# Kernel tuning notes

Measured on AMD Instinct MI355X. Metric: run time of the kernel, lower is better.

The kernel has to match this reference:

```python
import math
import jax, jax.numpy as jnp
import numpy as np

B, LD, LE = 8, 512, 512
D, H, DK, F, L, V = 1024, 16, 64, 4096, 3, 32000
EPS = 1e-5
NEG = -1000000000.0


def setup_inputs() -> dict:
    key = jax.random.key(0)
    ks = jax.random.split(key, 16)
    s = 0.02
    dec_inputs = jax.random.randint(ks[0], (B, LD), 0, V)
    # causal mask: True = masked out (matches masked_fill semantics)
    self_mask = jnp.broadcast_to(jnp.triu(jnp.ones((LD, LD), bool), k=1), (B, LD, LD))
    enc_output = jax.random.normal(ks[1], (B, LE, D), jnp.float32)
    encoder_mask = jnp.zeros((B, LD, LE), bool)  # no encoder padding
    embed = jax.random.normal(ks[2], (V, D), jnp.float32) * s
    # sinusoidal positional encoding, pe[:LD]
    pos = jnp.arange(LD, dtype=jnp.float32)[:, None]
    div = jnp.exp(jnp.arange(0, D, 2, dtype=jnp.float32) * (-math.log(10000.0) / D))
    pe = jnp.zeros((LD, D), jnp.float32)
    pe = pe.at[:, 0::2].set(jnp.sin(pos * div)).at[:, 1::2].set(jnp.cos(pos * div))
    # per-layer params; axis 1 of attn params: 0=self-attn, 1=enc-dec attn
    wq = jax.random.normal(ks[3], (L, 2, D, D), jnp.float32) * s
    wk = jax.random.normal(ks[4], (L, 2, D, D), jnp.float32) * s
    wv = jax.random.normal(ks[5], (L, 2, D, D), jnp.float32) * s
    wo = jax.random.normal(ks[6], (L, 2, D, D), jnp.float32) * s
    bq = jnp.zeros((L, 2, D), jnp.float32)
    bk = jnp.zeros((L, 2, D), jnp.float32)
    bv = jnp.zeros((L, 2, D), jnp.float32)
    bo = jnp.zeros((L, 2, D), jnp.float32)
    ffn_w1 = jax.random.normal(ks[7], (L, F, D), jnp.float32) * s
    ffn_b1 = jnp.zeros((L, F), jnp.float32)
    ffn_w2 = jax.random.normal(ks[8], (L, D, F), jnp.float32) * s
    ffn_b2 = jnp.zeros((L, D), jnp.float32)
    ln_g = jnp.ones((L, 3, D), jnp.float32)   # norm1/2/3 gains
    ln_b = jnp.zeros((L, 3, D), jnp.float32)  # norm1/2/3 biases
    return dict(dec_inputs=dec_inputs, self_mask=self_mask, enc_output=enc_output,
                encoder_mask=encoder_mask, embed=embed, pe=pe,
                wq=wq, bq=bq, wk=wk, bk=bk, wv=wv, bv=bv, wo=wo, bo=bo,
                ffn_w1=ffn_w1, ffn_b1=ffn_b1, ffn_w2=ffn_w2, ffn_b2=ffn_b2,
                ln_g=ln_g, ln_b=ln_b)


def _ln(x, g, b):
    m = jnp.mean(x, axis=-1, keepdims=True)
    v = jnp.mean((x - m) ** 2, axis=-1, keepdims=True)
    return (x - m) * jax.lax.rsqrt(v + EPS) * g + b


def _mha(qi, ki, vi, mask, wq, bq, wk, bk, wv, bv, wo, bo):
    Bq, Lq, _ = qi.shape
    Lk = ki.shape[1]
    Q = (qi @ wq.T + bq).reshape(Bq, Lq, H, DK).transpose(0, 2, 1, 3)
    K = (ki @ wk.T + bk).reshape(Bq, Lk, H, DK).transpose(0, 2, 1, 3)
    Vv = (vi @ wv.T + bv).reshape(Bq, Lk, H, DK).transpose(0, 2, 1, 3)
    scores = jnp.einsum('bhqd,bhkd->bhqk', Q, K) / math.sqrt(DK)
    scores = jnp.where(mask[:, None, :, :], NEG, scores)
    attn = jax.nn.softmax(scores, axis=-1)
    ctx = jnp.einsum('bhqk,bhkd->bhqd', attn, Vv)
    ctx = ctx.transpose(0, 2, 1, 3).reshape(Bq, Lq, H * DK)
    return ctx @ wo.T + bo


def reference(dec_inputs, self_mask, enc_output, encoder_mask, embed, pe,
              wq, bq, wk, bk, wv, bv, wo, bo,
              ffn_w1, ffn_b1, ffn_w2, ffn_b2, ln_g, ln_b):
    x = embed[dec_inputs] * math.sqrt(D) + pe[None, :, :]
    for l in range(L):
        h = _ln(x, ln_g[l, 0], ln_b[l, 0])
        a = _mha(h, h, h, self_mask,
                 wq[l, 0], bq[l, 0], wk[l, 0], bk[l, 0], wv[l, 0], bv[l, 0], wo[l, 0], bo[l, 0])
        x = x + a
        h = _ln(x, ln_g[l, 1], ln_b[l, 1])
        c = _mha(h, enc_output, enc_output, encoder_mask,
                 wq[l, 1], bq[l, 1], wk[l, 1], bk[l, 1], wv[l, 1], bv[l, 1], wo[l, 1], bo[l, 1])
        x = x + c
        h = _ln(x, ln_g[l, 2], ln_b[l, 2])
        f = jax.nn.relu(h @ ffn_w1[l].T + ffn_b1[l]) @ ffn_w2[l].T + ffn_b2[l]
        # faithful quirk of the source: residual is the cross-attn output, not x
        x = c + f
    return x
```

## Files before the change

### kernel.cpp

```cpp
#include <hip/hip_runtime.h>
#include <hip/hip_bf16.h>

using bf16x8 = __attribute__((ext_vector_type(8))) short;
using f32x4  = __attribute__((ext_vector_type(4))) float;
using u16x4  = __attribute__((ext_vector_type(4))) unsigned short;

#define DEVI static __device__ __forceinline__

DEVI unsigned short f2b(float f) {
  unsigned int u = __float_as_uint(f);
  u += 0x7FFFu + ((u >> 16) & 1u);
  return (unsigned short)(u >> 16);
}

DEVI void gload16(const unsigned short* g, unsigned short* l) {
  __builtin_amdgcn_global_load_lds(
      (const __attribute__((address_space(1))) unsigned int*)g,
      (__attribute__((address_space(3))) unsigned int*)l, 16, 0, 0);
}

DEVI float wred_max16(float v) {
#pragma unroll
  for (int m = 1; m < 16; m <<= 1) v = fmaxf(v, __shfl_xor(v, m, 64));
  return v;
}
DEVI float wred_sum16(float v) {
#pragma unroll
  for (int m = 1; m < 16; m <<= 1) v += __shfl_xor(v, m, 64);
  return v;
}


__global__ void cvt_kernel(const float* __restrict__ in,
                           unsigned short* __restrict__ out, int n4) {
  int i = blockIdx.x * blockDim.x + threadIdx.x;
  const int stride = gridDim.x * blockDim.x;
  for (; i < n4; i += stride) {
    const float4 v = ((const float4*)in)[i];
    u16x4 o;
    o[0] = f2b(v.x); o[1] = f2b(v.y); o[2] = f2b(v.z); o[3] = f2b(v.w);
    ((u16x4*)out)[i] = o;
  }
}

__global__ void pack_w(const float* __restrict__ s0,
                       const float* __restrict__ s1,
                       const float* __restrict__ s2,
                       int sub, unsigned short* __restrict__ dst, int nm) {
  const int r = blockIdx.x;
  const int m = blockIdx.y;
  const int l = blockIdx.z;
  const float* src = (m == 0 ? s0 : m == 1 ? s1 : s2)
                   + (size_t)(l * 2 + sub) * 1048576 + (size_t)r * 1024;
  unsigned short* d = dst + ((size_t)(l * nm + m) * 1024 + r) * 1024;
  const int col = threadIdx.x * 4;
  const float4 v = *(const float4*)(src + col);
  u16x4 o;
  o[0] = f2b(v.x); o[1] = f2b(v.y); o[2] = f2b(v.z); o[3] = f2b(v.w);
  *(u16x4*)(d + col) = o;
}

__global__ void pack_bias(const float* __restrict__ s0,
                          const float* __restrict__ s1,
                          const float* __restrict__ s2,
                          int sub, float* __restrict__ dst, int nm) {
  const int m = blockIdx.x, l = blockIdx.y;
  const float* src = (m == 0 ? s0 : m == 1 ? s1 : s2) + (size_t)(l * 2 + sub) * 1024;
  float* d = dst + ((size_t)l * nm + m) * 1024;
  const int i = threadIdx.x * 4;
  *(float4*)(d + i) = *(const float4*)(src + i);
}

__global__ void embed_kernel(const int* __restrict__ ids,
                             const float* __restrict__ emb,
                             const float* __restrict__ pe,
                             float* __restrict__ x) {
  const int row = blockIdx.x;
  const int t = row & 511;
  const int col = threadIdx.x * 4;
  const int id = ids[row];
  const float4 e = *(const float4*)(emb + (size_t)id * 1024 + col);
  const float4 p = *(const float4*)(pe + (size_t)t * 1024 + col);
  float4 o;
  o.x = e.x * 32.f + p.x; o.y = e.y * 32.f + p.y;
  o.z = e.z * 32.f + p.z; o.w = e.w * 32.f + p.w;
  *(float4*)(x + (size_t)row * 1024 + col) = o;
}

__global__ void ln_kernel(const float* __restrict__ x,
                          const float* __restrict__ g,
                          const float* __restrict__ b,
                          unsigned short* __restrict__ out) {
  const int row = blockIdx.x;
  const int l = threadIdx.x;
  const float4* xr = (const float4*)(x + (size_t)row * 1024);
  float4 v[4];
  float s = 0.f;
#pragma unroll
  for (int i = 0; i < 4; ++i) {
    v[i] = xr[l * 4 + i];
    s += v[i].x + v[i].y + v[i].z + v[i].w;
  }
#pragma unroll
  for (int m = 1; m < 64; m <<= 1) s += __shfl_xor(s, m, 64);
  const float mean = s * (1.f / 1024.f);
  float vs = 0.f;
#pragma unroll
  for (int i = 0; i < 4; ++i) {
    float dx = v[i].x - mean, dy = v[i].y - mean, dz = v[i].z - mean, dw = v[i].w - mean;
    vs += dx * dx + dy * dy + dz * dz + dw * dw;
  }
#pragma unroll
  for (int m = 1; m < 64; m <<= 1) vs += __shfl_xor(vs, m, 64);
  const float inv = rsqrtf(vs * (1.f / 1024.f) + 1e-5f);
#pragma unroll
  for (int i = 0; i < 4; ++i) {
    const int col = l * 16 + i * 4;
    const float4 gg = *(const float4*)(g + col);
    const float4 bb = *(const float4*)(b + col);
    u16x4 o;
    o[0] = f2b((v[i].x - mean) * inv * gg.x + bb.x);
    o[1] = f2b((v[i].y - mean) * inv * gg.y + bb.y);
    o[2] = f2b((v[i].z - mean) * inv * gg.z + bb.z);
    o[3] = f2b((v[i].w - mean) * inv * gg.w + bb.w);
    *(u16x4*)(out + (size_t)row * 1024 + col) = o;
  }
}


enum { EPI_BF16 = 0, EPI_RELU_BF16 = 1, EPI_RES = 2, EPI_RES2 = 3 };

template<int EPI>
__global__ void gemm_bt(const unsigned short* __restrict__ A,
                        const unsigned short* __restrict__ Bw,
                        const float* __restrict__ bias,
                        int N, int K, int nn,
                        void* out0, const float* res, float* out1) {
  __shared__ alignas(16) unsigned short As[2][64 * 64];
  __shared__ alignas(16) unsigned short Bs[2][128 * 64];
  const int tid = threadIdx.x;
  const int lane = tid & 63;
  const int wave = tid >> 6;
  int id = blockIdx.x;
  const int nwg = gridDim.x;
  id = (id & 7) * (nwg >> 3) + (id >> 3);
  const int bx = id % nn;
  const int by = id / nn;
  const int m0 = by * 64;
  const int n0 = bx * 128;
  const int wm = (wave >> 1) * 32;
  const int wn = (wave & 1) * 64;

  auto stage = [&](int buf, int kt) {
    const size_t k0 = (size_t)kt * 64;
#pragma unroll
    for (int i = 0; i < 2; ++i) {
      const int c = tid + 256 * i;
      const int row = c >> 3;
      const int lc = (c & 7) ^ (row & 7);
      gload16(A + (size_t)(m0 + row) * K + k0 + lc * 8, &As[buf][c * 8]);
    }
#pragma unroll
    for (int i = 0; i < 4; ++i) {
      const int c = tid + 256 * i;
      const int row = c >> 3;
      const int lc = (c & 7) ^ (row & 7);
      gload16(Bw + (size_t)(n0 + row) * K + k0 + lc * 8, &Bs[buf][c * 8]);
    }
  };

  f32x4 acc[2][4];
#pragma unroll
  for (int i = 0; i < 2; ++i)
#pragma unroll
    for (int j = 0; j < 4; ++j) acc[i][j] = f32x4{0.f, 0.f, 0.f, 0.f};

  const int nk = K >> 6;
  stage(0, 0);
  int cur = 0;
  const int ro = lane & 15;
  const int hi = lane >> 4;
  for (int kt = 0; kt < nk; ++kt) {
    __syncthreads();
    if (kt + 1 < nk) stage(cur ^ 1, kt + 1);
    bf16x8 af[2][2], bf[4][2];
#pragma unroll
    for (int i = 0; i < 2; ++i) {
      const int r = wm + i * 16 + ro;
#pragma unroll
      for (int ks = 0; ks < 2; ++ks)
        af[i][ks] = *(const bf16x8*)&As[cur][r * 64 + (((ks << 2) + hi) ^ (r & 7)) * 8];
    }
#pragma unroll
    for (int j = 0; j < 4; ++j) {
      const int r = wn + j * 16 + ro;
#pragma unroll
      for (int ks = 0; ks < 2; ++ks)
        bf[j][ks] = *(const bf16x8*)&Bs[cur][r * 64 + (((ks << 2) + hi) ^ (r & 7)) * 8];
    }
#pragma unroll
    for (int ks = 0; ks < 2; ++ks)
#pragma unroll
      for (int i = 0; i < 2; ++i)
#pragma unroll
        for (int j = 0; j < 4; ++j)
          acc[i][j] = __builtin_amdgcn_mfma_f32_16x16x32_bf16(af[i][ks], bf[j][ks], acc[i][j], 0, 0, 0);
    cur ^= 1;
  }

  const int r4 = hi * 4;
#pragma unroll
  for (int i = 0; i < 2; ++i) {
#pragma unroll
    for (int j = 0; j < 4; ++j) {
      const int cg = n0 + wn + j * 16 + ro;
      const float bv = bias[cg];
#pragma unroll
      for (int q = 0; q < 4; ++q) {
        const int rg = m0 + wm + i * 16 + r4 + q;
        const size_t idx = (size_t)rg * N + cg;
        const float v = acc[i][j][q] + bv;
        if (EPI == EPI_BF16) {
          ((unsigned short*)out0)[idx] = f2b(v);
        } else if (EPI == EPI_RELU_BF16) {
          ((unsigned short*)out0)[idx] = f2b(fmaxf(v, 0.f));
        } else if (EPI == EPI_RES) {
          ((float*)out0)[idx] = res[idx] + v;
        } else {
          const float r = res[idx];
          ((float*)out0)[idx] = v;
          out1[idx] = r + v;
        }
      }
    }
  }
}


template<bool CAUSAL>
__global__ __launch_bounds__(64) void attn_kernel(
    const unsigned short* __restrict__ Qg, int qs,
    const unsigned short* __restrict__ Kg, int ksd,
    const unsigned short* __restrict__ Vg, int vsd,
    unsigned short* __restrict__ Og) {
  __shared__ alignas(16) unsigned short Pl[64 * 64];
  const int qt = blockIdx.x;
  const int h  = blockIdx.y;
  const int b  = blockIdx.z;
  const int lane = threadIdx.x;
  const int ro = lane & 15;
  const int hi = lane >> 4;
  const size_t qbase = (size_t)b * 512 * qs  + (size_t)h * 64;
  const size_t kbase = (size_t)b * 512 * ksd + (size_t)h * 64;
  const size_t vbase = (size_t)b * 512 * vsd + (size_t)h * 64;
  const size_t obase = (size_t)b * 512 * 1024 + (size_t)h * 64;

  bf16x8 qf[4][2];
#pragma unroll
  for (int mi = 0; mi < 4; ++mi)
#pragma unroll
    for (int ks = 0; ks < 2; ++ks)
      qf[mi][ks] = *(const bf16x8*)&Qg[qbase + (size_t)(qt * 64 + mi * 16 + ro) * qs + ks * 32 + hi * 8];

  f32x4 o[4][4];
  float mrun[4][4], lrun[4][4];
#pragma unroll
  for (int mi = 0; mi < 4; ++mi) {
#pragma unroll
    for (int di = 0; di < 4; ++di) o[mi][di] = f32x4{0.f, 0.f, 0.f, 0.f};
#pragma unroll
    for (int q = 0; q < 4; ++q) { mrun[mi][q] = -1e30f; lrun[mi][q] = 0.f; }
  }

  const int ktmax = CAUSAL ? qt : 7;
  for (int kt = 0; kt <= ktmax; ++kt) {
    bf16x8 kf[4][2];
#pragma unroll
    for (int ni = 0; ni < 4; ++ni)
#pragma unroll
      for (int ks = 0; ks < 2; ++ks)
        kf[ni][ks] = *(const bf16x8*)&Kg[kbase + (size_t)(kt * 64 + ni * 16 + ro) * ksd + ks * 32 + hi * 8];

    f32x4 s[4][4];
#pragma unroll
    for (int mi = 0; mi < 4; ++mi)
#pragma unroll
      for (int ni = 0; ni < 4; ++ni) s[mi][ni] = f32x4{0.f, 0.f, 0.f, 0.f};
#pragma unroll
    for (int ks = 0; ks < 2; ++ks)
#pragma unroll
      for (int mi = 0; mi < 4; ++mi)
#pragma unroll
        for (int ni = 0; ni < 4; ++ni)
          s[mi][ni] = __builtin_amdgcn_mfma_f32_16x16x32_bf16(qf[mi][ks], kf[ni][ks], s[mi][ni], 0, 0, 0);

#pragma unroll
    for (int mi = 0; mi < 4; ++mi)
#pragma unroll
      for (int ni = 0; ni < 4; ++ni)
#pragma unroll
        for (int q = 0; q < 4; ++q) {
          float e = s[mi][ni][q] * 0.125f;
          if (CAUSAL && kt == qt && (ni * 16 + ro) > (mi * 16 + hi * 4 + q)) e = -1e9f;
          s[mi][ni][q] = e;
        }

    float fac[4][4];
#pragma unroll
    for (int mi = 0; mi < 4; ++mi)
#pragma unroll
      for (int q = 0; q < 4; ++q) {
        float rm = s[mi][0][q];
#pragma unroll
        for (int ni = 1; ni < 4; ++ni) rm = fmaxf(rm, s[mi][ni][q]);
        rm = wred_max16(rm);
        const float mn = fmaxf(mrun[mi][q], rm);
        fac[mi][q] = __expf(mrun[mi][q] - mn);
        mrun[mi][q] = mn;
      }
#pragma unroll
    for (int mi = 0; mi < 4; ++mi)
#pragma unroll
      for (int q = 0; q < 4; ++q) {
        float rs = 0.f;
#pragma unroll
        for (int ni = 0; ni < 4; ++ni) {
          const float pv = __expf(s[mi][ni][q] - mrun[mi][q]);
          s[mi][ni][q] = pv;
          rs += pv;
        }
        rs = wred_sum16(rs);
        lrun[mi][q] = lrun[mi][q] * fac[mi][q] + rs;
      }
#pragma unroll
    for (int mi = 0; mi < 4; ++mi)
#pragma unroll
      for (int di = 0; di < 4; ++di)
#pragma unroll
        for (int q = 0; q < 4; ++q) o[mi][di][q] *= fac[mi][q];

#pragma unroll
    for (int mi = 0; mi < 4; ++mi)
#pragma unroll
      for (int ni = 0; ni < 4; ++ni)
#pragma unroll
        for (int q = 0; q < 4; ++q)
          Pl[(mi * 16 + hi * 4 + q) * 64 + ni * 16 + ro] = f2b(s[mi][ni][q]);

    bf16x8 pa[4][2];
#pragma unroll
    for (int mi = 0; mi < 4; ++mi)
#pragma unroll
      for (int ks = 0; ks < 2; ++ks)
        pa[mi][ks] = *(const bf16x8*)&Pl[(mi * 16 + ro) * 64 + ks * 32 + hi * 8];

#pragma unroll
    for (int di = 0; di < 4; ++di)
#pragma unroll
      for (int ks = 0; ks < 2; ++ks) {
        bf16x8 vf;
#pragma unroll
        for (int jj = 0; jj < 8; ++jj)
          vf[jj] = (short)Vg[vbase + (size_t)(kt * 64 + ks * 32 + hi * 8 + jj) * vsd + di * 16 + ro];
#pragma unroll
        for (int mi = 0; mi < 4; ++mi)
          o[mi][di] = __builtin_amdgcn_mfma_f32_16x16x32_bf16(pa[mi][ks], vf, o[mi][di], 0, 0, 0);
      }
  }

#pragma unroll
  for (int mi = 0; mi < 4; ++mi)
#pragma unroll
    for (int di = 0; di < 4; ++di)
#pragma unroll
      for (int q = 0; q < 4; ++q) {
        const float val = o[mi][di][q] / lrun[mi][q];
        Og[obase + (size_t)(qt * 64 + mi * 16 + hi * 4 + q) * 1024 + di * 16 + ro] = f2b(val);
      }
}


extern "C" void kernel_launch(void* const* d_in, const int* in_sizes, int n_in,
                              void* d_out, int out_size, void* d_ws, size_t ws_size,
                              hipStream_t stream) {
  (void)in_sizes; (void)n_in; (void)out_size; (void)ws_size;
  const int*   dec = (const int*)d_in[0];
  const float* enc = (const float*)d_in[2];
  const float* emb = (const float*)d_in[4];
  const float* pe  = (const float*)d_in[5];
  const float* wq  = (const float*)d_in[6];
  const float* bq  = (const float*)d_in[7];
  const float* wk  = (const float*)d_in[8];
  const float* bk  = (const float*)d_in[9];
  const float* wv  = (const float*)d_in[10];
  const float* bv  = (const float*)d_in[11];
  const float* wo  = (const float*)d_in[12];
  const float* bo  = (const float*)d_in[13];
  const float* w1  = (const float*)d_in[14];
  const float* b1  = (const float*)d_in[15];
  const float* w2  = (const float*)d_in[16];
  const float* b2  = (const float*)d_in[17];
  const float* lng = (const float*)d_in[18];
  const float* lnb = (const float*)d_in[19];

  const size_t SZ_ACT = 4194304ull;

  char* p = (char*)d_ws;
  auto alloc = [&](size_t bytes) { char* r = p; p += (bytes + 255) & ~(size_t)255; return r; };
  unsigned short* qkvw  = (unsigned short*)alloc(3ull * 3 * 1048576 * 2);
  unsigned short* kvw   = (unsigned short*)alloc(3ull * 2 * 1048576 * 2);
  unsigned short* wqxb  = (unsigned short*)alloc(3ull * 1048576 * 2);
  unsigned short* Wob   = (unsigned short*)alloc(6291456ull * 2);
  unsigned short* W1b   = (unsigned short*)alloc(12582912ull * 2);
  unsigned short* W2b   = (unsigned short*)alloc(12582912ull * 2);
  unsigned short* encb  = (unsigned short*)alloc(SZ_ACT * 2);
  float*          x     = (float*)alloc(SZ_ACT * 4);
  float*          c     = (float*)alloc(SZ_ACT * 4);
  unsigned short* hb    = (unsigned short*)alloc(SZ_ACT * 2);
  unsigned short* qkvb  = (unsigned short*)alloc(4096ull * 3072 * 2);
  unsigned short* kvb   = (unsigned short*)alloc(4096ull * 2048 * 2);
  unsigned short* qb    = (unsigned short*)alloc(SZ_ACT * 2);
  unsigned short* mid   = (unsigned short*)alloc(4096ull * 4096 * 2);
  float*          qkvbias = (float*)alloc(3ull * 3072 * 4);
  float*          kvbias  = (float*)alloc(3ull * 2048 * 4);

  cvt_kernel<<<2048, 256, 0, stream>>>(wo, Wob, 1572864);
  cvt_kernel<<<2048, 256, 0, stream>>>(w1, W1b, 3145728);
  cvt_kernel<<<2048, 256, 0, stream>>>(w2, W2b, 3145728);
  cvt_kernel<<<2048, 256, 0, stream>>>(enc, encb, 1048576);
  pack_w<<<dim3(1024, 3, 3), 256, 0, stream>>>(wq, wk, wv, 0, qkvw, 3);
  pack_w<<<dim3(1024, 2, 3), 256, 0, stream>>>(wk, wv, wv, 1, kvw, 2);
  pack_w<<<dim3(1024, 1, 3), 256, 0, stream>>>(wq, wq, wq, 1, wqxb, 1);
  pack_bias<<<dim3(3, 3), 256, 0, stream>>>(bq, bk, bv, 0, qkvbias, 3);
  pack_bias<<<dim3(2, 3), 256, 0, stream>>>(bk, bv, bv, 1, kvbias, 2);
  embed_kernel<<<4096, 256, 0, stream>>>(dec, emb, pe, x);

  const dim3 gAttn(8, 16, 8);

  for (int l = 0; l < 3; ++l) {
    const float* g0 = lng + (l * 3 + 0) * 1024; const float* e0 = lnb + (l * 3 + 0) * 1024;
    const float* g1 = lng + (l * 3 + 1) * 1024; const float* e1 = lnb + (l * 3 + 1) * 1024;
    const float* g2 = lng + (l * 3 + 2) * 1024; const float* e2 = lnb + (l * 3 + 2) * 1024;

    ln_kernel<<<4096, 64, 0, stream>>>(x, g0, e0, hb);
    gemm_bt<EPI_BF16><<<64 * 24, 256, 0, stream>>>(hb, qkvw + (size_t)l * 3 * 1048576,
        qkvbias + l * 3072, 3072, 1024, 24, qkvb, nullptr, nullptr);
    attn_kernel<true><<<gAttn, 64, 0, stream>>>(qkvb, 3072, qkvb + 1024, 3072,
                                                qkvb + 2048, 3072, hb);
    gemm_bt<EPI_RES><<<64 * 8, 256, 0, stream>>>(hb, Wob + (size_t)(l * 2) * 1048576,
        bo + (l * 2) * 1024, 1024, 1024, 8, x, x, nullptr);

    ln_kernel<<<4096, 64, 0, stream>>>(x, g1, e1, hb);
    gemm_bt<EPI_BF16><<<64 * 8, 256, 0, stream>>>(hb, wqxb + (size_t)l * 1048576,
        bq + (l * 2 + 1) * 1024, 1024, 1024, 8, qb, nullptr, nullptr);
    gemm_bt<EPI_BF16><<<64 * 16, 256, 0, stream>>>(encb, kvw + (size_t)l * 2 * 1048576,
        kvbias + l * 2048, 2048, 1024, 16, kvb, nullptr, nullptr);
    attn_kernel<false><<<gAttn, 64, 0, stream>>>(qb, 1024, kvb, 2048, kvb + 1024, 2048, hb);
    gemm_bt<EPI_RES2><<<64 * 8, 256, 0, stream>>>(hb, Wob + (size_t)(l * 2 + 1) * 1048576,
        bo + (l * 2 + 1) * 1024, 1024, 1024, 8, c, x, x);

    ln_kernel<<<4096, 64, 0, stream>>>(x, g2, e2, hb);
    gemm_bt<EPI_RELU_BF16><<<64 * 32, 256, 0, stream>>>(hb, W1b + (size_t)l * 4194304,
        b1 + l * 4096, 4096, 1024, 32, mid, nullptr, nullptr);
    float* xout = (l == 2) ? (float*)d_out : x;
    gemm_bt<EPI_RES><<<64 * 8, 256, 0, stream>>>(mid, W2b + (size_t)l * 4194304,
        b2 + l * 1024, 1024, 4096, 8, xout, c, nullptr);
  }
}
```

Measured before the change: 1.265 ms.

## Pre-transpose V, halve attention query tile, and use narrower GEMM tiles for N=1024

```diff
diff --git a/kernel.cpp b/kernel.cpp
--- a/kernel.cpp
+++ b/kernel.cpp
@@ -127,17 +127,44 @@
   }
 }
 
+__global__ void vt_kernel(const unsigned short* __restrict__ Vsrc, int vsd,
+                          unsigned short* __restrict__ Vt) {
+  __shared__ alignas(16) unsigned short t[64][72];
+  const int tt = blockIdx.x;
+  const int h  = blockIdx.y;
+  const int b  = blockIdx.z;
+  const int tid = threadIdx.x;
+  const int r  = tid >> 2;
+  const int ch = tid & 3;
+  const unsigned short* src =
+      Vsrc + (size_t)(b * 512 + tt * 64 + r) * vsd + (size_t)h * 64 + ch * 16;
+  const bf16x8 v0 = *(const bf16x8*)src;
+  const bf16x8 v1 = *(const bf16x8*)(src + 8);
+#pragma unroll
+  for (int j = 0; j < 8; ++j) {
+    t[ch * 16 + j][r]     = (unsigned short)v0[j];
+    t[ch * 16 + 8 + j][r] = (unsigned short)v1[j];
+  }
+  __syncthreads();
+  const int d  = tid >> 2;
+  const int tp = tid & 3;
+  unsigned short* dst = Vt + (((size_t)(b * 16 + h) * 64 + d) * 512) + tt * 64 + tp * 16;
+  *(bf16x8*)dst       = *(const bf16x8*)&t[d][tp * 16];
+  *(bf16x8*)(dst + 8) = *(const bf16x8*)&t[d][tp * 16 + 8];
+}
+
 
 enum { EPI_BF16 = 0, EPI_RELU_BF16 = 1, EPI_RES = 2, EPI_RES2 = 3 };
 
-template<int EPI>
+template<int EPI, int BN>
 __global__ void gemm_bt(const unsigned short* __restrict__ A,
                         const unsigned short* __restrict__ Bw,
                         const float* __restrict__ bias,
                         int N, int K, int nn,
                         void* out0, const float* res, float* out1) {
+  constexpr int NJ = BN / 32;
   __shared__ alignas(16) unsigned short As[2][64 * 64];
-  __shared__ alignas(16) unsigned short Bs[2][128 * 64];
+  __shared__ alignas(16) unsigned short Bs[2][BN * 64];
   const int tid = threadIdx.x;
   const int lane = tid & 63;
   const int wave = tid >> 6;
@@ -147,9 +174,9 @@
   const int bx = id % nn;
   const int by = id / nn;
   const int m0 = by * 64;
-  const int n0 = bx * 128;
+  const int n0 = bx * BN;
   const int wm = (wave >> 1) * 32;
-  const int wn = (wave & 1) * 64;
+  const int wn = (wave & 1) * (BN / 2);
 
   auto stage = [&](int buf, int kt) {
     const size_t k0 = (size_t)kt * 64;
@@ -161,7 +188,7 @@
       gload16(A + (size_t)(m0 + row) * K + k0 + lc * 8, &As[buf][c * 8]);
     }
 #pragma unroll
-    for (int i = 0; i < 4; ++i) {
+    for (int i = 0; i < BN / 32; ++i) {
       const int c = tid + 256 * i;
       const int row = c >> 3;
       const int lc = (c & 7) ^ (row & 7);
@@ -169,11 +196,11 @@
     }
   };
 
-  f32x4 acc[2][4];
+  f32x4 acc[2][NJ];
 #pragma unroll
   for (int i = 0; i < 2; ++i)
 #pragma unroll
-    for (int j = 0; j < 4; ++j) acc[i][j] = f32x4{0.f, 0.f, 0.f, 0.f};
+    for (int j = 0; j < NJ; ++j) acc[i][j] = f32x4{0.f, 0.f, 0.f, 0.f};
 
   const int nk = K >> 6;
   stage(0, 0);
@@ -183,7 +210,7 @@
   for (int kt = 0; kt < nk; ++kt) {
     __syncthreads();
     if (kt + 1 < nk) stage(cur ^ 1, kt + 1);
-    bf16x8 af[2][2], bf[4][2];
+    bf16x8 af[2][2], bf[NJ][2];
 #pragma unroll
     for (int i = 0; i < 2; ++i) {
       const int r = wm + i * 16 + ro;
@@ -192,7 +219,7 @@
         af[i][ks] = *(const bf16x8*)&As[cur][r * 64 + (((ks << 2) + hi) ^ (r & 7)) * 8];
     }
 #pragma unroll
-    for (int j = 0; j < 4; ++j) {
+    for (int j = 0; j < NJ; ++j) {
       const int r = wn + j * 16 + ro;
 #pragma unroll
       for (int ks = 0; ks < 2; ++ks)
@@ -203,7 +230,7 @@
 #pragma unroll
       for (int i = 0; i < 2; ++i)
 #pragma unroll
-        for (int j = 0; j < 4; ++j)
+        for (int j = 0; j < NJ; ++j)
           acc[i][j] = __builtin_amdgcn_mfma_f32_16x16x32_bf16(af[i][ks], bf[j][ks], acc[i][j], 0, 0, 0);
     cur ^= 1;
   }
@@ -212,7 +239,7 @@
 #pragma unroll
   for (int i = 0; i < 2; ++i) {
 #pragma unroll
-    for (int j = 0; j < 4; ++j) {
+    for (int j = 0; j < NJ; ++j) {
       const int cg = n0 + wn + j * 16 + ro;
       const float bv = bias[cg];
 #pragma unroll
@@ -241,9 +268,9 @@
 __global__ __launch_bounds__(64) void attn_kernel(
     const unsigned short* __restrict__ Qg, int qs,
     const unsigned short* __restrict__ Kg, int ksd,
-    const unsigned short* __restrict__ Vg, int vsd,
+    const unsigned short* __restrict__ Vt,
     unsigned short* __restrict__ Og) {
-  __shared__ alignas(16) unsigned short Pl[64 * 64];
+  __shared__ alignas(16) unsigned short Pl[32 * 64];
   const int qt = blockIdx.x;
   const int h  = blockIdx.y;
   const int b  = blockIdx.z;
@@ -252,27 +279,27 @@
   const int hi = lane >> 4;
   const size_t qbase = (size_t)b * 512 * qs  + (size_t)h * 64;
   const size_t kbase = (size_t)b * 512 * ksd + (size_t)h * 64;
-  const size_t vbase = (size_t)b * 512 * vsd + (size_t)h * 64;
+  const size_t vbase = ((size_t)(b * 16 + h)) * 64 * 512;
   const size_t obase = (size_t)b * 512 * 1024 + (size_t)h * 64;
 
-  bf16x8 qf[4][2];
-#pragma unroll
-  for (int mi = 0; mi < 4; ++mi)
+  bf16x8 qf[2][2];
+#pragma unroll
+  for (int mi = 0; mi < 2; ++mi)
 #pragma unroll
     for (int ks = 0; ks < 2; ++ks)
-      qf[mi][ks] = *(const bf16x8*)&Qg[qbase + (size_t)(qt * 64 + mi * 16 + ro) * qs + ks * 32 + hi * 8];
-
-  f32x4 o[4][4];
-  float mrun[4][4], lrun[4][4];
-#pragma unroll
-  for (int mi = 0; mi < 4; ++mi) {
+      qf[mi][ks] = *(const bf16x8*)&Qg[qbase + (size_t)(qt * 32 + mi * 16 + ro) * qs + ks * 32 + hi * 8];
+
+  f32x4 o[2][4];
+  float mrun[2][4], lrun[2][4];
+#pragma unroll
+  for (int mi = 0; mi < 2; ++mi) {
 #pragma unroll
     for (int di = 0; di < 4; ++di) o[mi][di] = f32x4{0.f, 0.f, 0.f, 0.f};
 #pragma unroll
     for (int q = 0; q < 4; ++q) { mrun[mi][q] = -1e30f; lrun[mi][q] = 0.f; }
   }
 
-  const int ktmax = CAUSAL ? qt : 7;
+  const int ktmax = CAUSAL ? (qt >> 1) : 7;
   for (int kt = 0; kt <= ktmax; ++kt) {
     bf16x8 kf[4][2];
 #pragma unroll
@@ -281,33 +308,34 @@
       for (int ks = 0; ks < 2; ++ks)
         kf[ni][ks] = *(const bf16x8*)&Kg[kbase + (size_t)(kt * 64 + ni * 16 + ro) * ksd + ks * 32 + hi * 8];
 
-    f32x4 s[4][4];
-#pragma unroll
-    for (int mi = 0; mi < 4; ++mi)
+    f32x4 s[2][4];
+#pragma unroll
+    for (int mi = 0; mi < 2; ++mi)
 #pragma unroll
       for (int ni = 0; ni < 4; ++ni) s[mi][ni] = f32x4{0.f, 0.f, 0.f, 0.f};
 #pragma unroll
     for (int ks = 0; ks < 2; ++ks)
 #pragma unroll
-      for (int mi = 0; mi < 4; ++mi)
+      for (int mi = 0; mi < 2; ++mi)
 #pragma unroll
         for (int ni = 0; ni < 4; ++ni)
           s[mi][ni] = __builtin_amdgcn_mfma_f32_16x16x32_bf16(qf[mi][ks], kf[ni][ks], s[mi][ni], 0, 0, 0);
 
 #pragma unroll
-    for (int mi = 0; mi < 4; ++mi)
+    for (int mi = 0; mi < 2; ++mi)
 #pragma unroll
       for (int ni = 0; ni < 4; ++ni)
 #pragma unroll
         for (int q = 0; q < 4; ++q) {
           float e = s[mi][ni][q] * 0.125f;
-          if (CAUSAL && kt == qt && (ni * 16 + ro) > (mi * 16 + hi * 4 + q)) e = -1e9f;
+          if (CAUSAL && kt == ktmax &&
+              (kt * 64 + ni * 16 + ro) > (qt * 32 + mi * 16 + hi * 4 + q)) e = -1e9f;
           s[mi][ni][q] = e;
         }
 
-    float fac[4][4];
-#pragma unroll
-    for (int mi = 0; mi < 4; ++mi)
+    float fac[2][4];
+#pragma unroll
+    for (int mi = 0; mi < 2; ++mi)
 #pragma unroll
       for (int q = 0; q < 4; ++q) {
         float rm = s[mi][0][q];
@@ -319,7 +347,7 @@
         mrun[mi][q] = mn;
       }
 #pragma unroll
-    for (int mi = 0; mi < 4; ++mi)
+    for (int mi = 0; mi < 2; ++mi)
 #pragma unroll
       for (int q = 0; q < 4; ++q) {
         float rs = 0.f;
@@ -333,49 +361,52 @@
         lrun[mi][q] = lrun[mi][q] * fac[mi][q] + rs;
       }
 #pragma unroll
-    for (int mi = 0; mi < 4; ++mi)
+    for (int mi = 0; mi < 2; ++mi)
 #pragma unroll
       for (int di = 0; di < 4; ++di)
 #pragma unroll
         for (int q = 0; q < 4; ++q) o[mi][di][q] *= fac[mi][q];
 
 #pragma unroll
-    for (int mi = 0; mi < 4; ++mi)
+    for (int mi = 0; mi < 2; ++mi)
 #pragma unroll
       for (int ni = 0; ni < 4; ++ni)
 #pragma unroll
-        for (int q = 0; q < 4; ++q)
-          Pl[(mi * 16 + hi * 4 + q) * 64 + ni * 16 + ro] = f2b(s[mi][ni][q]);
-
-    bf16x8 pa[4][2];
-#pragma unroll
-    for (int mi = 0; mi < 4; ++mi)
-#pragma unroll
-      for (int ks = 0; ks < 2; ++ks)
-        pa[mi][ks] = *(const bf16x8*)&Pl[(mi * 16 + ro) * 64 + ks * 32 + hi * 8];
+        for (int q = 0; q < 4; ++q) {
+          const int row = mi * 16 + hi * 4 + q;
+          const int col = ni * 16 + ro;
+          const int sc  = ((col >> 3) ^ (row & 7)) * 8 + (col & 7);
+          Pl[row * 64 + sc] = f2b(s[mi][ni][q]);
+        }
+
+    bf16x8 pa[2][2];
+#pragma unroll
+    for (int mi = 0; mi < 2; ++mi)
+#pragma unroll
+      for (int ks = 0; ks < 2; ++ks) {
+        const int row = mi * 16 + ro;
+        pa[mi][ks] = *(const bf16x8*)&Pl[row * 64 + (((ks << 2) + hi) ^ (row & 7)) * 8];
+      }
 
 #pragma unroll
     for (int di = 0; di < 4; ++di)
 #pragma unroll
       for (int ks = 0; ks < 2; ++ks) {
-        bf16x8 vf;
-#pragma unroll
-        for (int jj = 0; jj < 8; ++jj)
-          vf[jj] = (short)Vg[vbase + (size_t)(kt * 64 + ks * 32 + hi * 8 + jj) * vsd + di * 16 + ro];
-#pragma unroll
-        for (int mi = 0; mi < 4; ++mi)
+        const bf16x8 vf = *(const bf16x8*)&Vt[vbase + (size_t)(di * 16 + ro) * 512 + kt * 64 + ks * 32 + hi * 8];
+#pragma unroll
+        for (int mi = 0; mi < 2; ++mi)
           o[mi][di] = __builtin_amdgcn_mfma_f32_16x16x32_bf16(pa[mi][ks], vf, o[mi][di], 0, 0, 0);
       }
   }
 
 #pragma unroll
-  for (int mi = 0; mi < 4; ++mi)
+  for (int mi = 0; mi < 2; ++mi)
 #pragma unroll
     for (int di = 0; di < 4; ++di)
 #pragma unroll
       for (int q = 0; q < 4; ++q) {
         const float val = o[mi][di][q] / lrun[mi][q];
-        Og[obase + (size_t)(qt * 64 + mi * 16 + hi * 4 + q) * 1024 + di * 16 + ro] = f2b(val);
+        Og[obase + (size_t)(qt * 32 + mi * 16 + hi * 4 + q) * 1024 + di * 16 + ro] = f2b(val);
       }
 }
 
@@ -420,6 +451,7 @@
   unsigned short* qkvb  = (unsigned short*)alloc(4096ull * 3072 * 2);
   unsigned short* kvb   = (unsigned short*)alloc(4096ull * 2048 * 2);
   unsigned short* qb    = (unsigned short*)alloc(SZ_ACT * 2);
+  unsigned short* vtb   = (unsigned short*)alloc(SZ_ACT * 2);
   unsigned short* mid   = (unsigned short*)alloc(4096ull * 4096 * 2);
   float*          qkvbias = (float*)alloc(3ull * 3072 * 4);
   float*          kvbias  = (float*)alloc(3ull * 2048 * 4);
@@ -435,7 +467,8 @@
   pack_bias<<<dim3(2, 3), 256, 0, stream>>>(bk, bv, bv, 1, kvbias, 2);
   embed_kernel<<<4096, 256, 0, stream>>>(dec, emb, pe, x);
 
-  const dim3 gAttn(8, 16, 8);
+  const dim3 gAttn(16, 16, 8);
+  const dim3 gVt(8, 16, 8);
 
   for (int l = 0; l < 3; ++l) {
     const float* g0 = lng + (l * 3 + 0) * 1024; const float* e0 = lnb + (l * 3 + 0) * 1024;
@@ -443,27 +476,28 @@
     const float* g2 = lng + (l * 3 + 2) * 1024; const float* e2 = lnb + (l * 3 + 2) * 1024;
 
     ln_kernel<<<4096, 64, 0, stream>>>(x, g0, e0, hb);
-    gemm_bt<EPI_BF16><<<64 * 24, 256, 0, stream>>>(hb, qkvw + (size_t)l * 3 * 1048576,
+    gemm_bt<EPI_BF16, 128><<<64 * 24, 256, 0, stream>>>(hb, qkvw + (size_t)l * 3 * 1048576,
         qkvbias + l * 3072, 3072, 1024, 24, qkvb, nullptr, nullptr);
-    attn_kernel<true><<<gAttn, 64, 0, stream>>>(qkvb, 3072, qkvb + 1024, 3072,
-                                                qkvb + 2048, 3072, hb);
-    gemm_bt<EPI_RES><<<64 * 8, 256, 0, stream>>>(hb, Wob + (size_t)(l * 2) * 1048576,
-        bo + (l * 2) * 1024, 1024, 1024, 8, x, x, nullptr);
+    vt_kernel<<<gVt, 256, 0, stream>>>(qkvb + 2048, 3072, vtb);
+    attn_kernel<true><<<gAttn, 64, 0, stream>>>(qkvb, 3072, qkvb + 1024, 3072, vtb, hb);
+    gemm_bt<EPI_RES, 64><<<64 * 16, 256, 0, stream>>>(hb, Wob + (size_t)(l * 2) * 1048576,
+        bo + (l * 2) * 1024, 1024, 1024, 16, x, x, nullptr);
 
     ln_kernel<<<4096, 64, 0, stream>>>(x, g1, e1, hb);
-    gemm_bt<EPI_BF16><<<64 * 8, 256, 0, stream>>>(hb, wqxb + (size_t)l * 1048576,
-        bq + (l * 2 + 1) * 1024, 1024, 1024, 8, qb, nullptr, nullptr);
-    gemm_bt<EPI_BF16><<<64 * 16, 256, 0, stream>>>(encb, kvw + (size_t)l * 2 * 1048576,
+    gemm_bt<EPI_BF16, 64><<<64 * 16, 256, 0, stream>>>(hb, wqxb + (size_t)l * 1048576,
+        bq + (l * 2 + 1) * 1024, 1024, 1024, 16, qb, nullptr, nullptr);
+    gemm_bt<EPI_BF16, 128><<<64 * 16, 256, 0, stream>>>(encb, kvw + (size_t)l * 2 * 1048576,
         kvbias + l * 2048, 2048, 1024, 16, kvb, nullptr, nullptr);
-    attn_kernel<false><<<gAttn, 64, 0, stream>>>(qb, 1024, kvb, 2048, kvb + 1024, 2048, hb);
-    gemm_bt<EPI_RES2><<<64 * 8, 256, 0, stream>>>(hb, Wob + (size_t)(l * 2 + 1) * 1048576,
-        bo + (l * 2 + 1) * 1024, 1024, 1024, 8, c, x, x);
+    vt_kernel<<<gVt, 256, 0, stream>>>(kvb + 1024, 2048, vtb);
+    attn_kernel<false><<<gAttn, 64, 0, stream>>>(qb, 1024, kvb, 2048, vtb, hb);
+    gemm_bt<EPI_RES2, 64><<<64 * 16, 256, 0, stream>>>(hb, Wob + (size_t)(l * 2 + 1) * 1048576,
+        bo + (l * 2 + 1) * 1024, 1024, 1024, 16, c, x, x);
 
     ln_kernel<<<4096, 64, 0, stream>>>(x, g2, e2, hb);
-    gemm_bt<EPI_RELU_BF16><<<64 * 32, 256, 0, stream>>>(hb, W1b + (size_t)l * 4194304,
+    gemm_bt<EPI_RELU_BF16, 128><<<64 * 32, 256, 0, stream>>>(hb, W1b + (size_t)l * 4194304,
         b1 + l * 4096, 4096, 1024, 32, mid, nullptr, nullptr);
     float* xout = (l == 2) ? (float*)d_out : x;
-    gemm_bt<EPI_RES><<<64 * 8, 256, 0, stream>>>(mid, W2b + (size_t)l * 4194304,
-        b2 + l * 1024, 1024, 4096, 8, xout, c, nullptr);
-  }
-}
+    gemm_bt<EPI_RES, 64><<<64 * 16, 256, 0, stream>>>(mid, W2b + (size_t)l * 4194304,
+        b2 + l * 1024, 1024, 4096, 16, xout, c, nullptr);
+  }
+}
```

Result: faster. 1.153 ms (-8.9%).
